# Kernel tuning notes

Measured on AMD Instinct MI355X. Metric: run time of the kernel, lower is better.

The kernel has to match this reference:

```python
import jax, jax.numpy as jnp
import numpy as np

# Config matching init_kwargs: input_shape=(512,512,28), stride=2
M, N, L = 512, 512, 28
STRIDE = 2
B = 8


def setup_inputs() -> dict:
    key = jax.random.key(0)
    kx, kp = jax.random.split(key)
    x = jax.random.normal(kx, (B, L, M, N), dtype=jnp.float32)
    # phi = (1 + sign(randn)) / 2  -> binary {0,1} mask of shape (M, N)
    phi = (jax.random.normal(kp, (M, N)) > 0).astype(jnp.float32)
    return {"x": x, "phi": phi}


def reference(x, phi):
    """CASSI forward: get_transpose(get_measurement(x, phi), phi, mask_mul=True).

    x:   (b, L, M, N) hyperspectral cube
    phi: (M, N) coded aperture, broadcast across L bands
    """
    b, l, m, n = x.shape
    n_out = n + STRIDE * (l - 1)

    # --- get_measurement: mask-multiply then per-band shift-and-accumulate ---
    y1 = x * phi[None, None, :, :]                      # (b, L, M, N)
    # column index each (band, col) lands in after dispersion shift
    scat_idx = (STRIDE * jnp.arange(l)[:, None] + jnp.arange(n)[None, :]).reshape(-1)  # (L*N,)
    y1f = y1.transpose(0, 2, 1, 3).reshape(b, m, l * n)  # (b, M, L*N)
    y2 = jnp.zeros((b, m, n_out), dtype=x.dtype).at[:, :, scat_idx].add(y1f)  # (b, M, Nout)
    # y_norm=False: no normalization

    # --- get_transpose: gather shifted windows (width = y.shape[-2] = M) ---
    gat_idx = STRIDE * jnp.arange(l)[:, None] + jnp.arange(m)[None, :]  # (L, M)
    xt = y2[:, :, gat_idx]             # (b, M, L, M)
    xt = jnp.moveaxis(xt, 2, 1)        # (b, L, M, M)
    return xt * phi[None, None, :, :]  # mask_mul=True
```

## Files before the change

### kernel.cpp

```cpp
#include <hip/hip_runtime.h>


#define M_DIM 512
#define N_DIM 512
#define L_DIM 28
#define B_DIM 8
#define MN_DIM (M_DIM * N_DIM)
#define NT 14
#define U_DIM 14
#define YSTRIDE 576
#define MB 8

typedef float v2f __attribute__((ext_vector_type(2)));
typedef float v4f __attribute__((ext_vector_type(4)));

__global__ __launch_bounds__(128) void cassi_y2_kernel(
    const float* __restrict__ x, const float* __restrict__ phi,
    float* __restrict__ y2w)
{
    __shared__ __align__(16) float sphi[N_DIM];

    const int t  = threadIdx.x;
    const int bm = blockIdx.x;
    const int b  = bm >> 9;
    const int m  = bm & 511;

    const float* xrow = x + (size_t)b * L_DIM * MN_DIM + (size_t)m * N_DIM;

    v4f pq = *(const v4f*)(phi + (size_t)m * N_DIM + 4 * t);
    *(v4f*)&sphi[4 * t] = pq;
    __syncthreads();

    const bool lane0 = ((t & 63) == 0);

    v4f acc  = {0.f, 0.f, 0.f, 0.f};
    v4f acct = {0.f, 0.f, 0.f, 0.f};

#pragma unroll
    for (int u = 0; u < U_DIM; ++u) {
        const int s  = t - u;
        const int sc = s < 0 ? 0 : s;
        const float* re = xrow + (size_t)(2 * u) * MN_DIM;
        const float* ro = xrow + (size_t)(2 * u + 1) * MN_DIM;
        v4f xe = *(const v4f*)(re + 4 * sc);
        v4f xo = *(const v4f*)(ro + 4 * sc);
        v4f P  = *(const v4f*)(&sphi[4 * sc]);
        v4f ze = xe * P;
        v4f zo = xo * P;

        if (s >= 0) acc += ze;

        float lo0 = __shfl_up(zo.z, 1, 64);
        float lo1 = __shfl_up(zo.w, 1, 64);
        if (lane0 && s >= 1) {
            v2f xl = *(const v2f*)(ro + 4 * s - 2);
            v2f pl = *(const v2f*)(&sphi[4 * s - 2]);
            lo0 = xl.x * pl.x;
            lo1 = xl.y * pl.y;
        }
        if (s >= 1) { acc.x += lo0;  acc.y += lo1; }
        if (s >= 0) { acc.z += zo.x; acc.w += zo.y; }

        if (t < NT) {
            if (u == t) {
                v2f xl = *(const v2f*)(ro + 510);
                v2f pl = *(const v2f*)(&sphi[510]);
                acct.x += xl.x * pl.x;
                acct.y += xl.y * pl.y;
            } else if (u > t) {
                const int n0 = 512 + 4 * t - 4 * u;
                v4f xte = *(const v4f*)(re + n0);
                v4f Pt  = *(const v4f*)(&sphi[n0]);
                acct += xte * Pt;
                v2f xa = *(const v2f*)(ro + n0 - 2);
                v2f pa = *(const v2f*)(&sphi[n0 - 2]);
                v2f xb = *(const v2f*)(ro + n0);
                acct.x += xa.x * pa.x;
                acct.y += xa.y * pa.y;
                acct.z += xb.x * Pt.x;
                acct.w += xb.y * Pt.y;
            }
        }
    }

    float* yrow = y2w + (size_t)bm * YSTRIDE;
    *(v4f*)(yrow + 4 * t) = acc;
    if (t < NT) *(v4f*)(yrow + 512 + 4 * t) = acct;
}

__global__ __launch_bounds__(256) void cassi_expand_kernel(
    const float* __restrict__ y2w, const float* __restrict__ phi,
    float* __restrict__ out)
{
    const int bid = blockIdx.x;
    const int mc  = bid & 63;
    const int bl  = bid >> 6;
    const int l   = bl % L_DIM;
    const int b   = bl / L_DIM;
    const int m0  = mc * MB;

    const int c = threadIdx.x & 31;
    const int r = threadIdx.x >> 5;
    const int m = m0 + r;

    const float* yrow = y2w + (size_t)((b << 9) | m) * YSTRIDE + 2 * l;
    const float* prow = phi + (size_t)m * N_DIM;
    float* orow = out + ((size_t)b * L_DIM + l) * MN_DIM + (size_t)m * N_DIM;

#pragma unroll
    for (int q = 0; q < 4; ++q) {
        const int n0 = 4 * c + 128 * q;
        v4f P  = *(const v4f*)(prow + n0);
        v2f ya = *(const v2f*)(yrow + n0);
        v2f yb = *(const v2f*)(yrow + n0 + 2);
        v4f o;
        o.x = P.x * ya.x;
        o.y = P.y * ya.y;
        o.z = P.z * yb.x;
        o.w = P.w * yb.y;
        __builtin_nontemporal_store(o, (v4f*)(orow + n0));
    }
}

__global__ __launch_bounds__(128) void cassi_fwd_kernel(
    const float* __restrict__ x, const float* __restrict__ phi,
    float* __restrict__ out)
{
    __shared__ __align__(16) float sphi[N_DIM];
    __shared__ __align__(16) float sy2[576];

    const int t  = threadIdx.x;
    const int bm = blockIdx.x;
    const int b  = bm >> 9;
    const int m  = bm & 511;

    const float* xrow = x + (size_t)b * L_DIM * MN_DIM + (size_t)m * N_DIM;

    v4f pq = *(const v4f*)(phi + (size_t)m * N_DIM + 4 * t);
    *(v4f*)&sphi[4 * t] = pq;
    __syncthreads();

    const bool lane0 = ((t & 63) == 0);
    v4f acc  = {0.f, 0.f, 0.f, 0.f};
    v4f acct = {0.f, 0.f, 0.f, 0.f};

#pragma unroll
    for (int u = 0; u < U_DIM; ++u) {
        const int s  = t - u;
        const int sc = s < 0 ? 0 : s;
        const float* re = xrow + (size_t)(2 * u) * MN_DIM;
        const float* ro = xrow + (size_t)(2 * u + 1) * MN_DIM;
        v4f xe = *(const v4f*)(re + 4 * sc);
        v4f xo = *(const v4f*)(ro + 4 * sc);
        v4f P  = *(const v4f*)(&sphi[4 * sc]);
        v4f ze = xe * P;
        v4f zo = xo * P;

        if (s >= 0) acc += ze;

        float lo0 = __shfl_up(zo.z, 1, 64);
        float lo1 = __shfl_up(zo.w, 1, 64);
        if (lane0 && s >= 1) {
            v2f xl = *(const v2f*)(ro + 4 * s - 2);
            v2f pl = *(const v2f*)(&sphi[4 * s - 2]);
            lo0 = xl.x * pl.x;
            lo1 = xl.y * pl.y;
        }
        if (s >= 1) { acc.x += lo0;  acc.y += lo1; }
        if (s >= 0) { acc.z += zo.x; acc.w += zo.y; }

        if (t < NT) {
            if (u == t) {
                v2f xl = *(const v2f*)(ro + 510);
                v2f pl = *(const v2f*)(&sphi[510]);
                acct.x += xl.x * pl.x;
                acct.y += xl.y * pl.y;
            } else if (u > t) {
                const int n0 = 512 + 4 * t - 4 * u;
                v4f xte = *(const v4f*)(re + n0);
                v4f Pt  = *(const v4f*)(&sphi[n0]);
                acct += xte * Pt;
                v2f xa = *(const v2f*)(ro + n0 - 2);
                v2f pa = *(const v2f*)(&sphi[n0 - 2]);
                v2f xb = *(const v2f*)(ro + n0);
                acct.x += xa.x * pa.x;
                acct.y += xa.y * pa.y;
                acct.z += xb.x * Pt.x;
                acct.w += xb.y * Pt.y;
            }
        }
    }

    *(v4f*)&sy2[4 * t] = acc;
    if (t < NT) *(v4f*)&sy2[512 + 4 * t] = acct;
    __syncthreads();

    float* orow = out + (size_t)b * L_DIM * MN_DIM + (size_t)m * N_DIM;
    const float* sy = &sy2[0];
#pragma unroll
    for (int l = 0; l < L_DIM; ++l) {
        v2f ya = *(const v2f*)(sy + 2 * l + 4 * t);
        v2f yb = *(const v2f*)(sy + 2 * l + 4 * t + 2);
        v4f o;
        o.x = pq.x * ya.x;
        o.y = pq.y * ya.y;
        o.z = pq.z * yb.x;
        o.w = pq.w * yb.y;
        __builtin_nontemporal_store(o, (v4f*)(orow + (size_t)l * MN_DIM + 4 * t));
    }
}

extern "C" void kernel_launch(void* const* d_in, const int* in_sizes, int n_in,
                              void* d_out, int out_size, void* d_ws, size_t ws_size,
                              hipStream_t stream) {
    const float* x   = (const float*)d_in[0];
    const float* phi = (const float*)d_in[1];
    float* out       = (float*)d_out;

    const size_t ws_needed = (size_t)B_DIM * M_DIM * YSTRIDE * sizeof(float);
    if (d_ws != nullptr && ws_size >= ws_needed) {
        float* y2w = (float*)d_ws;
        cassi_y2_kernel<<<dim3(B_DIM * M_DIM), dim3(128), 0, stream>>>(x, phi, y2w);
        cassi_expand_kernel<<<dim3(B_DIM * L_DIM * (M_DIM / MB)), dim3(256), 0, stream>>>(y2w, phi, out);
    } else {
        cassi_fwd_kernel<<<dim3(B_DIM * M_DIM), dim3(128), 0, stream>>>(x, phi, out);
    }
}
```

Baseline: 387.3 us.

## Restructure expand kernel to stage y2 rows in LDS and loop over all bands

```diff
diff --git a/kernel.cpp b/kernel.cpp
--- a/kernel.cpp
+++ b/kernel.cpp
@@ -88,37 +88,44 @@
     if (t < NT) *(v4f*)(yrow + 512 + 4 * t) = acct;
 }
 
-__global__ __launch_bounds__(256) void cassi_expand_kernel(
+__global__ __launch_bounds__(1024) void cassi_expand_kernel(
     const float* __restrict__ y2w, const float* __restrict__ phi,
     float* __restrict__ out)
 {
-    const int bid = blockIdx.x;
-    const int mc  = bid & 63;
-    const int bl  = bid >> 6;
-    const int l   = bl % L_DIM;
-    const int b   = bl / L_DIM;
-    const int m0  = mc * MB;
-
-    const int c = threadIdx.x & 31;
-    const int r = threadIdx.x >> 5;
+    __shared__ __align__(16) float sy[MB][YSTRIDE];
+
+    const int tid = threadIdx.x;
+    const int b   = blockIdx.x >> 6;
+    const int m0  = (blockIdx.x & 63) * MB;
+
+    {
+        const v4f* src = (const v4f*)(y2w + (size_t)((b << 9) | m0) * YSTRIDE);
+        v4f* dst = (v4f*)&sy[0][0];
+        dst[tid] = src[tid];
+        if (tid < 128) dst[1024 + tid] = src[1024 + tid];
+    }
+
+    const int r = tid >> 7;
+    const int t = tid & 127;
     const int m = m0 + r;
 
-    const float* yrow = y2w + (size_t)((b << 9) | m) * YSTRIDE + 2 * l;
-    const float* prow = phi + (size_t)m * N_DIM;
-    float* orow = out + ((size_t)b * L_DIM + l) * MN_DIM + (size_t)m * N_DIM;
-
-#pragma unroll
-    for (int q = 0; q < 4; ++q) {
-        const int n0 = 4 * c + 128 * q;
-        v4f P  = *(const v4f*)(prow + n0);
-        v2f ya = *(const v2f*)(yrow + n0);
-        v2f yb = *(const v2f*)(yrow + n0 + 2);
+    v4f pq = *(const v4f*)(phi + (size_t)m * N_DIM + 4 * t);
+
+    __syncthreads();
+
+    const float* syr = &sy[r][0];
+    float* oplane = out + (size_t)b * L_DIM * MN_DIM + (size_t)m * N_DIM + 4 * t;
+
+#pragma unroll
+    for (int l = 0; l < L_DIM; ++l) {
+        v2f ya = *(const v2f*)(syr + 2 * l + 4 * t);
+        v2f yb = *(const v2f*)(syr + 2 * l + 4 * t + 2);
         v4f o;
-        o.x = P.x * ya.x;
-        o.y = P.y * ya.y;
-        o.z = P.z * yb.x;
-        o.w = P.w * yb.y;
-        __builtin_nontemporal_store(o, (v4f*)(orow + n0));
+        o.x = pq.x * ya.x;
+        o.y = pq.y * ya.y;
+        o.z = pq.z * yb.x;
+        o.w = pq.w * yb.y;
+        __builtin_nontemporal_store(o, (v4f*)(oplane + (size_t)l * MN_DIM));
     }
 }
 
@@ -221,7 +228,7 @@
     if (d_ws != nullptr && ws_size >= ws_needed) {
         float* y2w = (float*)d_ws;
         cassi_y2_kernel<<<dim3(B_DIM * M_DIM), dim3(128), 0, stream>>>(x, phi, y2w);
-        cassi_expand_kernel<<<dim3(B_DIM * L_DIM * (M_DIM / MB)), dim3(256), 0, stream>>>(y2w, phi, out);
+        cassi_expand_kernel<<<dim3(B_DIM * (M_DIM / MB)), dim3(1024), 0, stream>>>(y2w, phi, out);
     } else {
         cassi_fwd_kernel<<<dim3(B_DIM * M_DIM), dim3(128), 0, stream>>>(x, phi, out);
     }
```

Measured after the change: 393.9 us. About the same (+1.7%).
